# Kernel tuning notes

Hardware: AMD Instinct MI355X
Metric: run time of the kernel (lower is better)

The kernel has to match this reference:

```python
import jax, jax.numpy as jnp
import numpy as np

NUM_ATOMS = 262144
INPUT_DIM = 256
HIDDEN_DIM = 256
NUM_HEADS = 8
HEAD_DIM = HIDDEN_DIM // NUM_HEADS
NUM_GRAPHS = 2048
SCALE = float(np.sqrt(HEAD_DIM))


def setup_inputs() -> dict:
    key = jax.random.key(0)
    ks = jax.random.split(key, 9)
    x = jax.random.normal(ks[0], (NUM_ATOMS, INPUT_DIM), dtype=jnp.float32)
    batch = jnp.sort(jax.random.randint(ks[1], (NUM_ATOMS,), 0, NUM_GRAPHS, dtype=jnp.int32))
    queries = jax.random.normal(ks[2], (NUM_HEADS, HEAD_DIM), dtype=jnp.float32)
    s_in = 1.0 / np.sqrt(INPUT_DIM)
    s_h = 1.0 / np.sqrt(HIDDEN_DIM)
    Wk = jax.random.uniform(ks[3], (INPUT_DIM, HIDDEN_DIM), jnp.float32, -s_in, s_in)
    bk = jax.random.uniform(ks[4], (HIDDEN_DIM,), jnp.float32, -s_in, s_in)
    Wv = jax.random.uniform(ks[5], (INPUT_DIM, HIDDEN_DIM), jnp.float32, -s_in, s_in)
    bv = jax.random.uniform(ks[6], (HIDDEN_DIM,), jnp.float32, -s_in, s_in)
    Wo = jax.random.uniform(ks[7], (HIDDEN_DIM, INPUT_DIM), jnp.float32, -s_h, s_h)
    bo = jax.random.uniform(ks[8], (INPUT_DIM,), jnp.float32, -s_h, s_h)
    return {"x": x, "batch": batch, "queries": queries, "Wk": Wk, "bk": bk,
            "Wv": Wv, "bv": bv, "Wo": Wo, "bo": bo}


def reference(x, batch, queries, Wk, bk, Wv, bv, Wo, bo):
    N = x.shape[0]
    # projections: [N, hidden] -> [N, H, D]
    keys = (x @ Wk + bk).reshape(N, NUM_HEADS, HEAD_DIM)
    values = (x @ Wv + bv).reshape(N, NUM_HEADS, HEAD_DIM)
    # per-node, per-head attention logits against learned queries
    scores = jnp.einsum('nhd,hd->nh', keys, queries) / SCALE  # [N, H]
    # segment-wise (per-graph) stable softmax over nodes
    seg_max = jax.ops.segment_max(scores, batch, num_segments=NUM_GRAPHS)  # [B, H]
    w = jnp.exp(scores - seg_max[batch])                                   # [N, H]
    denom = jax.ops.segment_sum(w, batch, num_segments=NUM_GRAPHS)         # [B, H]
    w = w / denom[batch]
    # weighted sum of values per graph: [B, H, D]
    attended = jax.ops.segment_sum(w[:, :, None] * values, batch, num_segments=NUM_GRAPHS)
    attended = attended.reshape(NUM_GRAPHS, HIDDEN_DIM)
    return attended @ Wo + bo  # [B, input_dim]
```

## Files before the change

### kernel.cpp

```cpp
#include <hip/hip_runtime.h>

#define N_ATOMS 262144
#define NGRAPH  2048
#define INV_SCALE 0.17677669529663687f

typedef float f32x2 __attribute__((ext_vector_type(2)));
typedef float f32x4 __attribute__((ext_vector_type(4)));

__device__ __forceinline__ f32x2 pk_mul(f32x2 a, f32x2 b) {
  f32x2 d; asm("v_pk_mul_f32 %0, %1, %2" : "=v"(d) : "v"(a), "v"(b)); return d;
}
__device__ __forceinline__ f32x2 pk_fma(f32x2 a, f32x2 b, f32x2 c) {
  f32x2 d; asm("v_pk_fma_f32 %0, %1, %2, %3" : "=v"(d) : "v"(a), "v"(b), "v"(c)); return d;
}
__device__ __forceinline__ f32x2 pk_fma_blo(f32x2 a, f32x2 b, f32x2 c) {
  f32x2 d; asm("v_pk_fma_f32 %0, %1, %2, %3 op_sel_hi:[0,1,1]"
               : "=v"(d) : "v"(a), "v"(b), "v"(c)); return d;
}
__device__ __forceinline__ f32x2 pk_fma_bhi(f32x2 a, f32x2 b, f32x2 c) {
  f32x2 d; asm("v_pk_fma_f32 %0, %1, %2, %3 op_sel:[1,0,0]"
               : "=v"(d) : "v"(a), "v"(b), "v"(c)); return d;
}

__global__ void k_prep(const float* __restrict__ Wk, const float* __restrict__ bk,
                       const float* __restrict__ q, float* __restrict__ P,
                       float* __restrict__ c) {
  int h = blockIdx.x, i = threadIdx.x;
  float s = 0.f;
  #pragma unroll
  for (int d = 0; d < 32; ++d)
    s = fmaf(Wk[i * 256 + h * 32 + d], q[h * 32 + d], s);
  P[h * 256 + i] = s;
  if (i == 0) {
    float cc = 0.f;
    #pragma unroll
    for (int d = 0; d < 32; ++d) cc = fmaf(bk[h * 32 + d], q[h * 32 + d], cc);
    c[h] = cc;
  }
}

__global__ void k_bounds(const int* __restrict__ batch, int* __restrict__ bounds) {
  int g = blockIdx.x * blockDim.x + threadIdx.x;
  if (g >= NGRAPH) return;
  int lo = 0, hi = N_ATOMS;
  while (lo < hi) {
    int mid = (lo + hi) >> 1;
    if (batch[mid] < g) lo = mid + 1; else hi = mid;
  }
  bounds[2 * g] = lo;
  if (g > 0) bounds[2 * g - 1] = lo;
  if (g == NGRAPH - 1) bounds[2 * g + 1] = N_ATOMS;
}

__device__ __forceinline__ float fold8(float acc[8], int lane) {
  {
    int m = lane & 8;
    float nw[4];
    #pragma unroll
    for (int j = 0; j < 4; ++j) {
      float snd = m ? acc[j] : acc[j + 4];
      float rcv = __shfl_xor(snd, 8, 64);
      nw[j] = (m ? acc[j + 4] : acc[j]) + rcv;
    }
    #pragma unroll
    for (int j = 0; j < 4; ++j) acc[j] = nw[j];
  }
  {
    int m = lane & 16;
    float nw[2];
    #pragma unroll
    for (int j = 0; j < 2; ++j) {
      float snd = m ? acc[j] : acc[j + 2];
      float rcv = __shfl_xor(snd, 16, 64);
      nw[j] = (m ? acc[j + 2] : acc[j]) + rcv;
    }
    acc[0] = nw[0]; acc[1] = nw[1];
  }
  float r;
  {
    int m = lane & 32;
    float snd = m ? acc[0] : acc[1];
    float rcv = __shfl_xor(snd, 32, 64);
    r = (m ? acc[1] : acc[0]) + rcv;
  }
  r += __shfl_xor(r, 1, 64);
  r += __shfl_xor(r, 2, 64);
  r += __shfl_xor(r, 4, 64);
  return r;
}

__global__ __launch_bounds__(256) void k_fused(const float* __restrict__ x,
                                               const float* __restrict__ P,
                                               const float* __restrict__ c,
                                               const int* __restrict__ bounds,
                                               float* __restrict__ Ag) {
  int b = blockIdx.x;
  int s = bounds[2 * b], e = bounds[2 * b + 1];
  int t = threadIdx.x, lane = t & 63, wv = t >> 6;
  int h = ((lane >> 1) & 4) | ((lane >> 3) & 2) | ((lane >> 5) & 1);

  f32x2 Pl2[8][2];
  #pragma unroll
  for (int k = 0; k < 8; ++k) {
    f32x4 pv = *reinterpret_cast<const f32x4*>(P + k * 256 + 4 * lane);
    Pl2[k][0] = __builtin_shufflevector(pv, pv, 0, 1);
    Pl2[k][1] = __builtin_shufflevector(pv, pv, 2, 3);
  }
  float cl = c[h];

  f32x2 A2[8][2];
  #pragma unroll
  for (int k = 0; k < 8; ++k) { A2[k][0] = (f32x2)0.f; A2[k][1] = (f32x2)0.f; }
  float dacc = 0.f;

  __shared__ float elds[4][2][8];

  for (int n0 = s + 2 * wv; n0 < e; n0 += 8) {
    bool has2 = (n0 + 1) < e;
    int n1 = has2 ? n0 + 1 : n0;
    f32x4 xq0 = *reinterpret_cast<const f32x4*>(x + (size_t)n0 * 256 + 4 * lane);
    f32x4 xq1 = *reinterpret_cast<const f32x4*>(x + (size_t)n1 * 256 + 4 * lane);
    f32x2 x0lo = __builtin_shufflevector(xq0, xq0, 0, 1);
    f32x2 x0hi = __builtin_shufflevector(xq0, xq0, 2, 3);
    f32x2 x1lo = __builtin_shufflevector(xq1, xq1, 0, 1);
    f32x2 x1hi = __builtin_shufflevector(xq1, xq1, 2, 3);

    float acc0[8], acc1[8];
    #pragma unroll
    for (int k = 0; k < 8; ++k) {
      f32x2 p0 = pk_fma(x0hi, Pl2[k][1], pk_mul(x0lo, Pl2[k][0]));
      f32x2 p1 = pk_fma(x1hi, Pl2[k][1], pk_mul(x1lo, Pl2[k][0]));
      acc0[k] = p0[0] + p0[1];
      acc1[k] = p1[0] + p1[1];
    }
    float r0 = fold8(acc0, lane);
    float r1 = fold8(acc1, lane);
    float ev0 = __expf((r0 + cl) * INV_SCALE);
    float ev1 = __expf((r1 + cl) * INV_SCALE);
    ev1 = has2 ? ev1 : 0.f;
    dacc += ev0 + ev1;

    if ((lane & 7) == 0) {
      elds[wv][0][h] = ev0;
      elds[wv][1][h] = ev1;
    }
    f32x4 ea03 = *reinterpret_cast<const f32x4*>(&elds[wv][0][0]);
    f32x4 ea47 = *reinterpret_cast<const f32x4*>(&elds[wv][0][4]);
    f32x4 eb03 = *reinterpret_cast<const f32x4*>(&elds[wv][1][0]);
    f32x4 eb47 = *reinterpret_cast<const f32x4*>(&elds[wv][1][4]);
    f32x2 ea[4] = { __builtin_shufflevector(ea03, ea03, 0, 1),
                    __builtin_shufflevector(ea03, ea03, 2, 3),
                    __builtin_shufflevector(ea47, ea47, 0, 1),
                    __builtin_shufflevector(ea47, ea47, 2, 3) };
    f32x2 eb[4] = { __builtin_shufflevector(eb03, eb03, 0, 1),
                    __builtin_shufflevector(eb03, eb03, 2, 3),
                    __builtin_shufflevector(eb47, eb47, 0, 1),
                    __builtin_shufflevector(eb47, eb47, 2, 3) };
    #pragma unroll
    for (int j = 0; j < 4; ++j) {
      A2[2*j][0]   = pk_fma_blo(ea[j], x0lo, A2[2*j][0]);
      A2[2*j][1]   = pk_fma_blo(ea[j], x0hi, A2[2*j][1]);
      A2[2*j+1][0] = pk_fma_bhi(ea[j], x0lo, A2[2*j+1][0]);
      A2[2*j+1][1] = pk_fma_bhi(ea[j], x0hi, A2[2*j+1][1]);
      A2[2*j][0]   = pk_fma_blo(eb[j], x1lo, A2[2*j][0]);
      A2[2*j][1]   = pk_fma_blo(eb[j], x1hi, A2[2*j][1]);
      A2[2*j+1][0] = pk_fma_bhi(eb[j], x1lo, A2[2*j+1][0]);
      A2[2*j+1][1] = pk_fma_bhi(eb[j], x1hi, A2[2*j+1][1]);
    }
  }

  __shared__ float As[4][8][256];
  __shared__ float dws[4][8];
  __shared__ float dinvs[8];
  #pragma unroll
  for (int k = 0; k < 8; ++k) {
    float4 av;
    av.x = A2[k][0][0]; av.y = A2[k][0][1];
    av.z = A2[k][1][0]; av.w = A2[k][1][1];
    *reinterpret_cast<float4*>(&As[wv][k][4 * lane]) = av;
  }
  if ((lane & 7) == 0) dws[wv][h] = dacc;
  __syncthreads();
  if (t < 8) {
    float ds = dws[0][t] + dws[1][t] + dws[2][t] + dws[3][t];
    dinvs[t] = ds > 0.f ? 1.0f / ds : 0.f;
  }
  __syncthreads();
  #pragma unroll
  for (int r2 = 0; r2 < 8; ++r2) {
    float v = As[0][r2][t] + As[1][r2][t] + As[2][r2][t] + As[3][r2][t];
    Ag[(size_t)b * 2048 + r2 * 256 + t] = v * dinvs[r2];
  }
}

__global__ __launch_bounds__(256) void k_out(const float* __restrict__ Ag,
                                             const int* __restrict__ bounds,
                                             const float* __restrict__ Wv,
                                             const float* __restrict__ bv,
                                             const float* __restrict__ Wo,
                                             const float* __restrict__ bo,
                                             float* __restrict__ out) {
  __shared__ float Alds[4 * 2048];
  __shared__ float attlds[4 * 256];
  __shared__ float eflag[4];
  int b0 = blockIdx.x * 4;
  int t = threadIdx.x;
  #pragma unroll
  for (int r = 0; r < 32; ++r) {
    int idx = r * 256 + t;
    Alds[idx] = Ag[(size_t)b0 * 2048 + idx];
  }
  if (t < 4) {
    int s = bounds[2 * (b0 + t)], e = bounds[2 * (b0 + t) + 1];
    eflag[t] = (e > s) ? 1.0f : 0.0f;
  }
  __syncthreads();
  int h = t >> 5;
  float bvk = bv[t];
  float acc[4];
  #pragma unroll
  for (int g = 0; g < 4; ++g) acc[g] = 0.f;
  for (int i4 = 0; i4 < 64; ++i4) {
    float aa[4][4];
    #pragma unroll
    for (int g = 0; g < 4; ++g) {
      float4 v = *reinterpret_cast<const float4*>(&Alds[g * 2048 + h * 256 + i4 * 4]);
      aa[g][0] = v.x; aa[g][1] = v.y; aa[g][2] = v.z; aa[g][3] = v.w;
    }
    #pragma unroll
    for (int j = 0; j < 4; ++j) {
      float wvv = Wv[(size_t)(i4 * 4 + j) * 256 + t];
      #pragma unroll
      for (int g = 0; g < 4; ++g) acc[g] = fmaf(aa[g][j], wvv, acc[g]);
    }
  }
  #pragma unroll
  for (int g = 0; g < 4; ++g) attlds[g * 256 + t] = acc[g] + bvk * eflag[g];
  __syncthreads();
  float boj = bo[t];
  float o[4];
  #pragma unroll
  for (int g = 0; g < 4; ++g) o[g] = boj;
  for (int k4 = 0; k4 < 64; ++k4) {
    float aa[4][4];
    #pragma unroll
    for (int g = 0; g < 4; ++g) {
      float4 v = *reinterpret_cast<const float4*>(&attlds[g * 256 + k4 * 4]);
      aa[g][0] = v.x; aa[g][1] = v.y; aa[g][2] = v.z; aa[g][3] = v.w;
    }
    #pragma unroll
    for (int j = 0; j < 4; ++j) {
      float wo = Wo[(size_t)(k4 * 4 + j) * 256 + t];
      #pragma unroll
      for (int g = 0; g < 4; ++g) o[g] = fmaf(aa[g][j], wo, o[g]);
    }
  }
  #pragma unroll
  for (int g = 0; g < 4; ++g) out[(size_t)(b0 + g) * 256 + t] = o[g];
}

extern "C" void kernel_launch(void* const* d_in, const int* in_sizes, int n_in,
                              void* d_out, int out_size, void* d_ws, size_t ws_size,
                              hipStream_t stream) {
  const float* x   = (const float*)d_in[0];
  const int*   bat = (const int*)d_in[1];
  const float* q   = (const float*)d_in[2];
  const float* Wk  = (const float*)d_in[3];
  const float* bk  = (const float*)d_in[4];
  const float* Wv  = (const float*)d_in[5];
  const float* bv  = (const float*)d_in[6];
  const float* Wo  = (const float*)d_in[7];
  const float* bo  = (const float*)d_in[8];
  float* out = (float*)d_out;

  float* ws = (float*)d_ws;
  float* P      = ws;
  float* c      = ws + 2048;
  int*   bounds = (int*)(ws + 4096);
  float* Ag     = ws + 8192;

  k_prep<<<8, 256, 0, stream>>>(Wk, bk, q, P, c);
  k_bounds<<<8, 256, 0, stream>>>(bat, bounds);
  k_fused<<<NGRAPH, 256, 0, stream>>>(x, P, c, bounds, Ag);
  k_out<<<NGRAPH / 4, 256, 0, stream>>>(Ag, bounds, Wv, bv, Wo, bo, out);
}
```

Baseline: 103.0 us.

## Merge prep kernels, shrink fused-kernel LDS reduction buffer, use nontemporal x loads

Merges the P/c precompute and segment-bounds binary search into one launch to save a kernel launch. In the fused attention kernel, the 32 KB shared buffer for the cross-wave reduction becomes an 8 KB buffer processed in four rounds. This is meant to raise occupancy, at the cost of extra barriers. The streaming loads of x now use nontemporal hints to avoid polluting cache.

```diff
diff --git a/kernel.cpp b/kernel.cpp
--- a/kernel.cpp
+++ b/kernel.cpp
@@ -21,35 +21,39 @@
   f32x2 d; asm("v_pk_fma_f32 %0, %1, %2, %3 op_sel:[1,0,0]"
                : "=v"(d) : "v"(a), "v"(b), "v"(c)); return d;
 }
-
-__global__ void k_prep(const float* __restrict__ Wk, const float* __restrict__ bk,
-                       const float* __restrict__ q, float* __restrict__ P,
-                       float* __restrict__ c) {
-  int h = blockIdx.x, i = threadIdx.x;
-  float s = 0.f;
-  #pragma unroll
-  for (int d = 0; d < 32; ++d)
-    s = fmaf(Wk[i * 256 + h * 32 + d], q[h * 32 + d], s);
-  P[h * 256 + i] = s;
-  if (i == 0) {
-    float cc = 0.f;
-    #pragma unroll
-    for (int d = 0; d < 32; ++d) cc = fmaf(bk[h * 32 + d], q[h * 32 + d], cc);
-    c[h] = cc;
-  }
-}
-
-__global__ void k_bounds(const int* __restrict__ batch, int* __restrict__ bounds) {
-  int g = blockIdx.x * blockDim.x + threadIdx.x;
-  if (g >= NGRAPH) return;
-  int lo = 0, hi = N_ATOMS;
-  while (lo < hi) {
-    int mid = (lo + hi) >> 1;
-    if (batch[mid] < g) lo = mid + 1; else hi = mid;
-  }
-  bounds[2 * g] = lo;
-  if (g > 0) bounds[2 * g - 1] = lo;
-  if (g == NGRAPH - 1) bounds[2 * g + 1] = N_ATOMS;
+__device__ __forceinline__ f32x4 ldnt4(const float* p) {
+  return __builtin_nontemporal_load(reinterpret_cast<const f32x4*>(p));
+}
+
+__global__ void k_pre(const float* __restrict__ Wk, const float* __restrict__ bk,
+                      const float* __restrict__ q, const int* __restrict__ batch,
+                      float* __restrict__ P, float* __restrict__ c,
+                      int* __restrict__ bounds) {
+  if (blockIdx.x < 8) {
+    int h = blockIdx.x, i = threadIdx.x;
+    float s = 0.f;
+    #pragma unroll
+    for (int d = 0; d < 32; ++d)
+      s = fmaf(Wk[i * 256 + h * 32 + d], q[h * 32 + d], s);
+    P[h * 256 + i] = s;
+    if (i == 0) {
+      float cc = 0.f;
+      #pragma unroll
+      for (int d = 0; d < 32; ++d) cc = fmaf(bk[h * 32 + d], q[h * 32 + d], cc);
+      c[h] = cc;
+    }
+  } else {
+    int g = (blockIdx.x - 8) * 256 + threadIdx.x;
+    if (g >= NGRAPH) return;
+    int lo = 0, hi = N_ATOMS;
+    while (lo < hi) {
+      int mid = (lo + hi) >> 1;
+      if (batch[mid] < g) lo = mid + 1; else hi = mid;
+    }
+    bounds[2 * g] = lo;
+    if (g > 0) bounds[2 * g - 1] = lo;
+    if (g == NGRAPH - 1) bounds[2 * g + 1] = N_ATOMS;
+  }
 }
 
 __device__ __forceinline__ float fold8(float acc[8], int lane) {
@@ -114,12 +118,15 @@
   float dacc = 0.f;
 
   __shared__ float elds[4][2][8];
+  __shared__ float Asc[4][2][256];
+  __shared__ float dws[4][8];
+  __shared__ float dinvs[8];
 
   for (int n0 = s + 2 * wv; n0 < e; n0 += 8) {
     bool has2 = (n0 + 1) < e;
     int n1 = has2 ? n0 + 1 : n0;
-    f32x4 xq0 = *reinterpret_cast<const f32x4*>(x + (size_t)n0 * 256 + 4 * lane);
-    f32x4 xq1 = *reinterpret_cast<const f32x4*>(x + (size_t)n1 * 256 + 4 * lane);
+    f32x4 xq0 = ldnt4(x + (size_t)n0 * 256 + 4 * lane);
+    f32x4 xq1 = ldnt4(x + (size_t)n1 * 256 + 4 * lane);
     f32x2 x0lo = __builtin_shufflevector(xq0, xq0, 0, 1);
     f32x2 x0hi = __builtin_shufflevector(xq0, xq0, 2, 3);
     f32x2 x1lo = __builtin_shufflevector(xq1, xq1, 0, 1);
@@ -169,27 +176,27 @@
     }
   }
 
-  __shared__ float As[4][8][256];
-  __shared__ float dws[4][8];
-  __shared__ float dinvs[8];
-  #pragma unroll
-  for (int k = 0; k < 8; ++k) {
-    float4 av;
-    av.x = A2[k][0][0]; av.y = A2[k][0][1];
-    av.z = A2[k][1][0]; av.w = A2[k][1][1];
-    *reinterpret_cast<float4*>(&As[wv][k][4 * lane]) = av;
-  }
   if ((lane & 7) == 0) dws[wv][h] = dacc;
   __syncthreads();
   if (t < 8) {
     float ds = dws[0][t] + dws[1][t] + dws[2][t] + dws[3][t];
     dinvs[t] = ds > 0.f ? 1.0f / ds : 0.f;
   }
-  __syncthreads();
-  #pragma unroll
-  for (int r2 = 0; r2 < 8; ++r2) {
-    float v = As[0][r2][t] + As[1][r2][t] + As[2][r2][t] + As[3][r2][t];
-    Ag[(size_t)b * 2048 + r2 * 256 + t] = v * dinvs[r2];
+  #pragma unroll
+  for (int p = 0; p < 4; ++p) {
+    float4 a0, a1;
+    a0.x = A2[2*p][0][0];   a0.y = A2[2*p][0][1];
+    a0.z = A2[2*p][1][0];   a0.w = A2[2*p][1][1];
+    a1.x = A2[2*p+1][0][0]; a1.y = A2[2*p+1][0][1];
+    a1.z = A2[2*p+1][1][0]; a1.w = A2[2*p+1][1][1];
+    *reinterpret_cast<float4*>(&Asc[wv][0][4 * lane]) = a0;
+    *reinterpret_cast<float4*>(&Asc[wv][1][4 * lane]) = a1;
+    __syncthreads();
+    float v0 = Asc[0][0][t] + Asc[1][0][t] + Asc[2][0][t] + Asc[3][0][t];
+    float v1 = Asc[0][1][t] + Asc[1][1][t] + Asc[2][1][t] + Asc[3][1][t];
+    Ag[(size_t)b * 2048 + (2*p) * 256 + t]   = v0 * dinvs[2*p];
+    Ag[(size_t)b * 2048 + (2*p+1) * 256 + t] = v1 * dinvs[2*p+1];
+    __syncthreads();
   }
 }
 
@@ -279,8 +286,7 @@
   int*   bounds = (int*)(ws + 4096);
   float* Ag     = ws + 8192;
 
-  k_prep<<<8, 256, 0, stream>>>(Wk, bk, q, P, c);
-  k_bounds<<<8, 256, 0, stream>>>(bat, bounds);
+  k_pre<<<16, 256, 0, stream>>>(Wk, bk, q, bat, P, c, bounds);
   k_fused<<<NGRAPH, 256, 0, stream>>>(x, P, c, bounds, Ag);
   k_out<<<NGRAPH / 4, 256, 0, stream>>>(Ag, bounds, Wv, bv, Wo, bo, out);
 }
```

After: 98.03 us. -4.8%, faster.
